# Kernel tuning notes

Hardware: AMD Instinct MI355X
Metric: run time of the kernel (lower is better)

Reference implementation:

```python
import jax, jax.numpy as jnp
import numpy as np
import math

B, T, N, IN_FEAT = 2, 64, 128, 2
H_LSTM = IN_FEAT * 2   # 4
D = IN_FEAT * 4        # 8
FH, FW = 16, 16
C_MAP = 2048
C_COMP = 32
TH = 0.5
IMG = 512.0


def setup_inputs() -> dict:
    key = jax.random.key(0)
    ks = jax.random.split(key, 20)
    s = 0.02
    inp = {
        "x": jax.random.uniform(ks[0], (B, 2, T, N), jnp.float32) * IMG,  # pixel coords in [0,512)
        "metadata": jax.random.normal(ks[1], (B, C_MAP, FH, FW), jnp.float32),
        # LSTM(in_feat, 2*in_feat): gates order i,f,g,o
        "w_ih": jax.random.normal(ks[2], (4 * H_LSTM, IN_FEAT), jnp.float32) * s,
        "w_hh": jax.random.normal(ks[3], (4 * H_LSTM, H_LSTM), jnp.float32) * s,
        "b_ih": jax.random.normal(ks[4], (4 * H_LSTM,), jnp.float32) * s,
        "b_hh": jax.random.normal(ks[5], (4 * H_LSTM,), jnp.float32) * s,
        "fc_w": jax.random.normal(ks[6], (D, H_LSTM), jnp.float32) * s,
        "fc_b": jax.random.normal(ks[7], (D,), jnp.float32) * s,
        "fc2_w": jax.random.normal(ks[8], (D, IN_FEAT), jnp.float32) * s,
        "fc2_b": jax.random.normal(ks[9], (D,), jnp.float32) * s,
        "fc3_w": jax.random.normal(ks[10], (D, IN_FEAT), jnp.float32) * s,
        "fc3_b": jax.random.normal(ks[11], (D,), jnp.float32) * s,
        "comp_w": jax.random.normal(ks[12], (C_COMP, C_MAP), jnp.float32) * s,
        "comp_b": jax.random.normal(ks[13], (C_COMP,), jnp.float32) * s,
        "vf_w": jax.random.normal(ks[14], (H_LSTM, H_LSTM + C_COMP), jnp.float32) * s,
        "vf_b": jax.random.normal(ks[15], (H_LSTM,), jnp.float32) * s,
        "fcout_w": jax.random.normal(ks[16], (IN_FEAT, D), jnp.float32) * s,
        "fcout_b": jax.random.normal(ks[17], (IN_FEAT,), jnp.float32) * s,
    }
    return inp


def _grid_sample_bilinear(fm, grid):
    # fm: [B,C,H,W]; grid: [B,P,1,2] normalized (x,y) in [-1,1]; bilinear, zeros padding, align_corners=False
    Bb, C, Hh, Ww = fm.shape
    gx, gy = grid[..., 0], grid[..., 1]              # [B,P,1]
    ix = ((gx + 1.0) * Ww - 1.0) * 0.5
    iy = ((gy + 1.0) * Hh - 1.0) * 0.5
    ix0 = jnp.floor(ix); iy0 = jnp.floor(iy)
    wx = ix - ix0; wy = iy - iy0

    def gather(f, yy, xx):
        valid = ((yy >= 0) & (yy < Hh) & (xx >= 0) & (xx < Ww)).astype(f.dtype)
        yc = jnp.clip(yy, 0, Hh - 1).astype(jnp.int32)
        xc = jnp.clip(xx, 0, Ww - 1).astype(jnp.int32)
        return f[:, yc, xc] * valid[None]            # [C,P,1]

    def per_batch(f, x0, y0, wx_, wy_):
        x1 = x0 + 1.0; y1 = y0 + 1.0
        return (gather(f, y0, x0) * ((1 - wy_) * (1 - wx_))[None]
                + gather(f, y0, x1) * ((1 - wy_) * wx_)[None]
                + gather(f, y1, x0) * (wy_ * (1 - wx_))[None]
                + gather(f, y1, x1) * (wy_ * wx_)[None])

    return jax.vmap(per_batch)(fm, ix0, iy0, wx, wy)  # [B,C,P,1]


def reference(x, metadata, w_ih, w_hh, b_ih, b_hh, fc_w, fc_b, fc2_w, fc2_b,
              fc3_w, fc3_b, comp_w, comp_b, vf_w, vf_b, fcout_w, fcout_b):
    coords = x                                        # [B,2,T,N] raw pixel coords
    xp = jnp.transpose(x, (0, 2, 3, 1))               # [B,T,N,2]
    b, t, n, c = xp.shape

    # sinusoidal positional encoding over time axis
    div = jnp.exp(jnp.arange(0, c, 2, dtype=jnp.float32) * (-math.log(10000.0) / c))
    pos = jnp.arange(t, dtype=jnp.float32)[:, None]
    pe = jnp.zeros((t, c), xp.dtype)
    pe = pe.at[:, 0::2].set(jnp.sin(pos * div))
    pe = pe.at[:, 1::2].set(jnp.cos(pos * div))
    xp = xp + pe[None, :, None, :]
    xr = xp.reshape(-1, c)                            # [M,2], M=b*t*n

    # single-step LSTM with zero init state (seq_len==1 in original)
    gates = xr @ w_ih.T + b_ih + b_hh                 # h0=0 => W_hh term vanishes
    i, f, g, o = jnp.split(gates, 4, axis=-1)
    cst = jax.nn.sigmoid(i) * jnp.tanh(g)
    X = jax.nn.sigmoid(o) * jnp.tanh(cst)             # [M,4]

    # visual fusion: 1x1 conv compressor + grid_sample local context
    comp = jnp.einsum('bchw,oc->bohw', metadata, comp_w) + comp_b[None, :, None, None]
    cgrid = jnp.transpose(coords, (0, 2, 3, 1)).reshape(b, -1, 1, 2)
    ngrid = 2.0 * (cgrid / IMG) - 1.0
    sampled = _grid_sample_bilinear(comp, ngrid)      # [B,32,TN,1]
    lc = jnp.transpose(sampled[..., 0], (0, 2, 1)).reshape(-1, C_COMP)  # [M,32]
    X = jnp.concatenate([X, lc], axis=-1) @ vf_w.T + vf_b               # [M,4]

    # sigmoid-gated full attention over all t*n tokens
    Q = (X @ fc_w.T + fc_b).reshape(b, t * n, -1)     # [B,TN,8]
    K = (xr @ fc2_w.T + fc2_b).reshape(b, t * n, -1)
    V = (xr @ fc3_w.T + fc3_b).reshape(b, t * n, -1)
    probs = jax.nn.sigmoid(jnp.einsum('bqd,bkd->bqk', Q, K))  # [B,TN,TN]
    out = jnp.einsum('bqk,bkd->bqd', probs, V).reshape(-1, Q.shape[-1])

    out = out * (out > TH).astype(out.dtype)          # threshold-ReLU
    out = out @ fcout_w.T + fcout_b                   # [M,2]
    out = out.reshape(b, t, n, -1)
    return jnp.transpose(out, (0, 3, 1, 2))           # [B,2,T,N]
```

## Files before the change

### kernel.cpp

```cpp
#include <hip/hip_runtime.h>
#include <math.h>

#define BB    2
#define TT    64
#define NN    128
#define TN    8192
#define MM    16384
#define CMAP  2048
#define CCOMP 32
#define FHW   256

#define CSPLIT 64
#define CRANGE 32

#define DEG    17
#define NS     18
#define NODD   9
#define MDIM   19
#define NMOMF  (MDIM*MDIM)
#define MCH    64
#define MPTS   128
#define ZFIT   5.0
#define ZFITF  5.0f
#define UVBOUND 1.0045f

struct QCoef { float cb[NS][NODD]; };

#define OFF_CP    0
#define OFF_COMP  (OFF_CP + CSPLIT*BB*FHW*CCOMP)
#define OFF_A     (OFF_COMP + BB*FHW*CCOMP)
#define OFF_X     (OFF_A + MM*4)
#define OFF_MP    (OFF_X + MM*2)

__device__ __forceinline__ float fast_sigmoid(float v) {
    return __builtin_amdgcn_rcpf(1.0f + __expf(-v));
}
__device__ __forceinline__ float fast_tanh(float v) {
    return 1.0f - 2.0f * __builtin_amdgcn_rcpf(1.0f + __expf(2.0f * v));
}

__global__ void k_comp_p(const float* __restrict__ metadata,
                         const float* __restrict__ comp_w,
                         float* __restrict__ Cp) {
    const int b  = blockIdx.x;
    const int cs = blockIdx.y;
    const int hw = threadIdx.x;

    __shared__ float wcs[CRANGE][CCOMP];
    for (int i = threadIdx.x; i < CRANGE * CCOMP; i += 256) {
        int c = i / CCOMP, o = i % CCOMP;
        wcs[c][o] = comp_w[o * CMAP + cs * CRANGE + c];
    }
    __syncthreads();

    float acc[CCOMP];
#pragma unroll
    for (int o = 0; o < CCOMP; o++) acc[o] = 0.0f;

    const float* mb = metadata + ((size_t)b * CMAP + (size_t)cs * CRANGE) * FHW + hw;
#pragma unroll 4
    for (int c = 0; c < CRANGE; c++) {
        float m = mb[c * FHW];
#pragma unroll
        for (int o = 0; o < CCOMP; o++) acc[o] += m * wcs[c][o];
    }

    float* outp = Cp + (size_t)cs * (BB * FHW * CCOMP) + ((size_t)b * FHW + hw) * CCOMP;
#pragma unroll
    for (int o = 0; o < CCOMP; o += 4) {
        *(float4*)&outp[o] = make_float4(acc[o], acc[o + 1], acc[o + 2], acc[o + 3]);
    }
}

__global__ void k_comp_reduce(const float* __restrict__ Cp,
                              const float* __restrict__ comp_b,
                              float* __restrict__ comp_ws) {
    const int t = threadIdx.x;
    const int i = blockIdx.x * 64 + (t >> 2);
    const int r = t & 3;

    float s = 0.0f;
#pragma unroll
    for (int k = 0; k < CSPLIT / 4; k++) {
        s += Cp[(size_t)(r * (CSPLIT / 4) + k) * (BB * FHW * CCOMP) + i];
    }
    s += __shfl_xor(s, 1);
    s += __shfl_xor(s, 2);
    if (r == 0) comp_ws[i] = s + comp_b[i & (CCOMP - 1)];
}

__global__ void k_token(const float* __restrict__ x,
                        const float* __restrict__ w_ih,
                        const float* __restrict__ b_ih,
                        const float* __restrict__ b_hh,
                        const float* __restrict__ fc_w,  const float* __restrict__ fc_b,
                        const float* __restrict__ fc2_w, const float* __restrict__ fc2_b,
                        const float* __restrict__ vf_w,  const float* __restrict__ vf_b,
                        const float* __restrict__ comp_ws,
                        float4* __restrict__ Aq, float2* __restrict__ Xr) {
    const int m = blockIdx.x * 64 + threadIdx.x;
    const int b = m >> 13;
    const int p = m & (TN - 1);
    const int t = p >> 7;

    const float px = x[(size_t)(b * 2 + 0) * TN + p];
    const float py = x[(size_t)(b * 2 + 1) * TN + p];

    const float xr0 = px + __sinf((float)t);
    const float xr1 = py + __cosf((float)t);
    Xr[m] = make_float2(xr0, xr1);

    float X[4];
#pragma unroll
    for (int j = 0; j < 4; j++) {
        float gi = xr0 * w_ih[(j)      * 2] + xr1 * w_ih[(j)      * 2 + 1] + b_ih[j]      + b_hh[j];
        float gg = xr0 * w_ih[(8 + j)  * 2] + xr1 * w_ih[(8 + j)  * 2 + 1] + b_ih[8 + j]  + b_hh[8 + j];
        float go = xr0 * w_ih[(12 + j) * 2] + xr1 * w_ih[(12 + j) * 2 + 1] + b_ih[12 + j] + b_hh[12 + j];
        float cst = fast_sigmoid(gi) * fast_tanh(gg);
        X[j] = fast_sigmoid(go) * fast_tanh(cst);
    }

    float lc[CCOMP];
#pragma unroll
    for (int c = 0; c < CCOMP; c++) lc[c] = 0.0f;

    const float ix = px * (1.0f / 32.0f) - 0.5f;
    const float iy = py * (1.0f / 32.0f) - 0.5f;
    const float fx0 = floorf(ix), fy0 = floorf(iy);
    const float wx = ix - fx0, wy = iy - fy0;
    const int x0 = (int)fx0, y0 = (int)fy0;
    const float* cb = comp_ws + (size_t)b * FHW * CCOMP;

#pragma unroll
    for (int dy = 0; dy < 2; dy++) {
#pragma unroll
        for (int dx = 0; dx < 2; dx++) {
            int xx = x0 + dx, yy = y0 + dy;
            if (xx < 0 || xx > 15 || yy < 0 || yy > 15) continue;
            float w = (dy ? wy : 1.0f - wy) * (dx ? wx : 1.0f - wx);
            const float4* cp4 = (const float4*)(cb + (yy * 16 + xx) * CCOMP);
#pragma unroll
            for (int c4 = 0; c4 < CCOMP / 4; c4++) {
                float4 v = cp4[c4];
                lc[c4 * 4 + 0] += w * v.x;
                lc[c4 * 4 + 1] += w * v.y;
                lc[c4 * 4 + 2] += w * v.z;
                lc[c4 * 4 + 3] += w * v.w;
            }
        }
    }

    float X2[4];
#pragma unroll
    for (int j = 0; j < 4; j++) {
        float a = vf_b[j];
#pragma unroll
        for (int k = 0; k < 4; k++) a += X[k] * vf_w[j * 36 + k];
#pragma unroll
        for (int c = 0; c < CCOMP; c++) a += lc[c] * vf_w[j * 36 + 4 + c];
        X2[j] = a;
    }

    float al = 0.0f, be = 0.0f, ga = 0.0f;
#pragma unroll
    for (int d = 0; d < 8; d++) {
        float q = fc_b[d];
#pragma unroll
        for (int k = 0; k < 4; k++) q += X2[k] * fc_w[d * 4 + k];
        al += q * fc2_b[d];
        be += q * fc2_w[d * 2];
        ga += q * fc2_w[d * 2 + 1];
    }
    Aq[m] = make_float4(al, be, ga, 0.0f);
}

__global__ void __launch_bounds__(256) k_mom(const float2* __restrict__ Xr,
                                             float* __restrict__ Mp) {
    const int b   = blockIdx.x;
    const int ch  = blockIdx.y;
    const int tid = threadIdx.x;

    __shared__ float spu[MPTS][MDIM];
    __shared__ float spv[MPTS][MDIM];

    if (tid < MPTS) {
        float2 xv = Xr[b * TN + ch * MPTS + tid];
        const float u = (xv.x - 256.0f) * (1.0f / 256.0f);
        const float v = (xv.y - 256.0f) * (1.0f / 256.0f);
        float a = 1.0f, c = 1.0f;
#pragma unroll
        for (int i = 0; i < MDIM; i++) {
            spu[tid][i] = a; spv[tid][i] = c;
            a *= u; c *= v;
        }
    }
    __syncthreads();

    float* outp = Mp + ((size_t)(b * MCH + ch)) * NMOMF;
    for (int i = tid; i < NMOMF; i += 256) {
        const int j = i / MDIM, l = i % MDIM;
        float s = 0.0f;
        if (j + l < MDIM) {
#pragma unroll 8
            for (int p = 0; p < MPTS; p++)
                s += spu[p][j] * spv[p][l];
        }
        outp[i] = s;
    }
}

__global__ void __launch_bounds__(256) k_query(const float4* __restrict__ Aq,
                                               const float2* __restrict__ Xr,
                                               const float* __restrict__ Mp,
                                               const float* __restrict__ fc3_w,
                                               const float* __restrict__ fc3_b,
                                               const float* __restrict__ fcout_w,
                                               const float* __restrict__ fcout_b,
                                               float* __restrict__ y,
                                               QCoef qc) {
    __shared__ float sM[NMOMF];

    const int tid = threadIdx.x;
    const int m   = blockIdx.x * 256 + tid;
    const int b   = m >> 13;
    const int p   = m & (TN - 1);

    for (int i = tid; i < NMOMF; i += 256) {
        float s = 0.0f;
        for (int ch = 0; ch < MCH; ch++)
            s += Mp[((size_t)(b * MCH + ch)) * NMOMF + i];
        sM[i] = s;
    }
    __syncthreads();

    const float4 A4 = Aq[m];
    const float al = A4.x, be = A4.y, ga = A4.z;
    const float b1 = 256.0f * be;
    const float c1 = 256.0f * ga;
    const float a0 = al + 256.0f * (be + ga);

    float S0, S1, S2;
    const float zb = fabsf(a0) + UVBOUND * (fabsf(b1) + fabsf(c1));
    if (zb >= ZFITF) {
        float s0 = 0.0f, s1 = 0.0f, s2 = 0.0f;
        const float2* xp = Xr + b * TN;
        for (int k = 0; k < TN; k++) {
            float2 kv = xp[k];
            float z = al + be * kv.x + ga * kv.y;
            float sg = fast_sigmoid(z);
            s0 += sg; s1 += sg * kv.x; s2 += sg * kv.y;
        }
        S0 = s0; S1 = s1; S2 = s2;
    } else {
        float pa[NS];
        pa[0] = 1.0f;
#pragma unroll
        for (int t = 1; t < NS; t++) pa[t] = pa[t - 1] * a0;

        float A[NS];
#pragma unroll
        for (int s = 0; s < NS; s++) {
            float acc = 0.0f;
            const int t0 = (s & 1) ? 0 : 1;
#pragma unroll
            for (int q = 0; q < NODD; q++) {
                const int t = t0 + 2 * q;
                if (s + t <= DEG) acc = fmaf(qc.cb[s][q], pa[t], acc);
            }
            A[s] = acc;
        }

        float R0 = A[0] * sM[0];
        float R1 = A[0] * sM[1 * MDIM + 0];
        float R2 = A[0] * sM[0 * MDIM + 1];

        float Ep[NS], Ec[NS];
        Ep[0] = 1.0f;
#pragma unroll
        for (int s = 1; s < NS; s++) {
            Ec[0] = c1 * Ep[0];
#pragma unroll
            for (int j = 1; j < NS; j++)
                if (j < s) Ec[j] = fmaf(b1, Ep[j - 1], c1 * Ep[j]);
            Ec[s] = b1 * Ep[s - 1];

            float W = 0.0f, W1 = 0.0f, W2 = 0.0f;
#pragma unroll
            for (int j = 0; j < NS; j++) {
                if (j <= s) {
                    const int l = s - j;
                    const float e = Ec[j];
                    W  = fmaf(e, sM[j * MDIM + l],           W);
                    W1 = fmaf(e, sM[(j + 1) * MDIM + l],     W1);
                    W2 = fmaf(e, sM[j * MDIM + l + 1],       W2);
                }
            }
            R0 = fmaf(A[s], W,  R0);
            R1 = fmaf(A[s], W1, R1);
            R2 = fmaf(A[s], W2, R2);
#pragma unroll
            for (int j = 0; j < NS; j++)
                if (j <= s) Ep[j] = Ec[j];
        }

        S0 = 4096.0f + R0;
        const float su = 0.5f * sM[1 * MDIM + 0] + R1;
        const float sv = 0.5f * sM[0 * MDIM + 1] + R2;
        S1 = 256.0f * su + 256.0f * S0;
        S2 = 256.0f * sv + 256.0f * S0;
    }

    float f0 = fcout_b[0], f1 = fcout_b[1];
#pragma unroll
    for (int d = 0; d < 8; d++) {
        float vv = S0 * fc3_b[d] + S1 * fc3_w[d * 2] + S2 * fc3_w[d * 2 + 1];
        vv = (vv > 0.5f) ? vv : 0.0f;
        f0 += vv * fcout_w[d];
        f1 += vv * fcout_w[8 + d];
    }
    y[(size_t)(b * 2 + 0) * TN + p] = f0;
    y[(size_t)(b * 2 + 1) * TN + p] = f1;
}

static QCoef compute_qcoef() {
    const int NNODE = 64;
    const double PI = 3.14159265358979323846;
    double term[NODD];
    for (int i = 0; i < NODD; ++i) term[i] = 0.0;

    for (int jn = 0; jn < NNODE; ++jn) {
        double theta = (jn + 0.5) * (PI / NNODE);
        double ct = cos(theta);
        double zj = ZFIT * ct;
        double fj = 1.0 / (1.0 + exp(-zj)) - 0.5;
        double Ckm2 = 1.0, Ckm1 = ct;
        term[0] += fj * ct;
        int idx = 1;
        for (int k = 2; k <= DEG; ++k) {
            double Ck = 2.0 * ct * Ckm1 - Ckm2;
            Ckm2 = Ckm1; Ckm1 = Ck;
            if (k & 1) term[idx++] += fj * Ck;
        }
    }

    double c[DEG + 1];
    for (int i = 0; i <= DEG; ++i) c[i] = 0.0;
    for (int i = 0; i < NODD; ++i) c[2 * i + 1] = term[i] * (2.0 / NNODE);

    double Tm2[DEG + 1], Tm1[DEG + 1], a[DEG + 1];
    for (int i = 0; i <= DEG; ++i) { Tm2[i] = 0.0; Tm1[i] = 0.0; a[i] = 0.0; }
    Tm2[0] = 1.0; Tm1[1] = 1.0;
    a[1] = c[1];
    for (int k = 2; k <= DEG; ++k) {
        double Tc[DEG + 1];
        for (int mm = 0; mm <= DEG; ++mm) Tc[mm] = 0.0;
        for (int mm = 0; mm <= k; ++mm) {
            double vv = -Tm2[mm];
            if (mm > 0) vv += 2.0 * Tm1[mm - 1];
            Tc[mm] = vv;
        }
        if (k & 1)
            for (int mm = 1; mm <= k; mm += 2) a[mm] += c[k] * Tc[mm];
        for (int mm = 0; mm <= DEG; ++mm) { Tm2[mm] = Tm1[mm]; Tm1[mm] = Tc[mm]; }
    }

    double Cz[DEG + 1];
    double sc = 1.0;
    for (int mm = 0; mm <= DEG; ++mm) { Cz[mm] = a[mm] * sc; sc *= (1.0 / ZFIT); }

    double Bi[NS][NS];
    for (int n = 0; n < NS; ++n)
        for (int k = 0; k < NS; ++k) Bi[n][k] = 0.0;
    for (int n = 0; n < NS; ++n) {
        Bi[n][0] = 1.0;
        for (int k = 1; k <= n; ++k)
            Bi[n][k] = Bi[n - 1][k - 1] + ((k <= n - 1) ? Bi[n - 1][k] : 0.0);
    }

    QCoef qc;
    for (int s = 0; s < NS; ++s)
        for (int q = 0; q < NODD; ++q) qc.cb[s][q] = 0.0f;
    for (int s = 0; s < NS; ++s) {
        int q = 0;
        for (int t = (s & 1) ? 0 : 1; s + t <= DEG; t += 2)
            qc.cb[s][q++] = (float)(Cz[s + t] * Bi[s + t][s]);
    }
    return qc;
}

extern "C" void kernel_launch(void* const* d_in, const int* in_sizes, int n_in,
                              void* d_out, int out_size, void* d_ws, size_t ws_size,
                              hipStream_t stream) {
    const float* x        = (const float*)d_in[0];
    const float* metadata = (const float*)d_in[1];
    const float* w_ih     = (const float*)d_in[2];
    const float* b_ih     = (const float*)d_in[4];
    const float* b_hh     = (const float*)d_in[5];
    const float* fc_w     = (const float*)d_in[6];
    const float* fc_b     = (const float*)d_in[7];
    const float* fc2_w    = (const float*)d_in[8];
    const float* fc2_b    = (const float*)d_in[9];
    const float* fc3_w    = (const float*)d_in[10];
    const float* fc3_b    = (const float*)d_in[11];
    const float* comp_w   = (const float*)d_in[12];
    const float* comp_b   = (const float*)d_in[13];
    const float* vf_w     = (const float*)d_in[14];
    const float* vf_b     = (const float*)d_in[15];
    const float* fcout_w  = (const float*)d_in[16];
    const float* fcout_b  = (const float*)d_in[17];

    static const QCoef qc = compute_qcoef();

    float*  ws      = (float*)d_ws;
    float*  Cp      = ws + OFF_CP;
    float*  comp_ws = ws + OFF_COMP;
    float4* Aq      = (float4*)(ws + OFF_A);
    float2* Xr      = (float2*)(ws + OFF_X);
    float*  Mp      = ws + OFF_MP;

    k_comp_p<<<dim3(BB, CSPLIT), 256, 0, stream>>>(metadata, comp_w, Cp);

    k_comp_reduce<<<256, 256, 0, stream>>>(Cp, comp_b, comp_ws);

    k_token<<<MM / 64, 64, 0, stream>>>(x, w_ih, b_ih, b_hh,
                                        fc_w, fc_b, fc2_w, fc2_b,
                                        vf_w, vf_b, comp_ws, Aq, Xr);

    k_mom<<<dim3(BB, MCH), 256, 0, stream>>>(Xr, Mp);

    k_query<<<MM / 256, 256, 0, stream>>>(Aq, Xr, Mp, fc3_w, fc3_b,
                                          fcout_w, fcout_b, (float*)d_out, qc);
}
```

Before: 127.0 us.

## Fuse all stages into one persistent kernel with software grid barriers

Replaces the five separate launches (compressor partials, reduction, per-token, moments, query) with a single 64-block persistent kernel. Phases are separated by atomic-counter grid barriers, and the per-token projections stay in registers instead of going through the Aq workspace buffer. The channel split and moment chunking are retuned to fit 64 blocks of 256 threads. This removes launch gaps and one global round-trip, but runs each phase on only 64 workgroups, adds barrier spin cost, and relies on all blocks being co-resident.

New measurement: 149.1 us. +17.4%, slower.

```diff
diff --git a/kernel.cpp b/kernel.cpp
--- a/kernel.cpp
+++ b/kernel.cpp
@@ -10,16 +10,18 @@
 #define CCOMP 32
 #define FHW   256
 
-#define CSPLIT 64
-#define CRANGE 32
+#define NBLK   64
+#define NTHR   256
+#define CSPLIT 32
+#define CRANGE 64
 
 #define DEG    17
 #define NS     18
 #define NODD   9
 #define MDIM   19
 #define NMOMF  (MDIM*MDIM)
-#define MCH    64
-#define MPTS   128
+#define MCH    32
+#define MPTS   256
 #define ZFIT   5.0
 #define ZFITF  5.0f
 #define UVBOUND 1.0045f
@@ -28,9 +30,24 @@
 
 #define OFF_CP    0
 #define OFF_COMP  (OFF_CP + CSPLIT*BB*FHW*CCOMP)
-#define OFF_A     (OFF_COMP + BB*FHW*CCOMP)
-#define OFF_X     (OFF_A + MM*4)
+#define OFF_X     (OFF_COMP + BB*FHW*CCOMP)
 #define OFF_MP    (OFF_X + MM*2)
+
+#define NBAR 4
+__device__ unsigned g_bar[NBAR];
+
+__device__ __forceinline__ void grid_bar(int ph) {
+    __syncthreads();
+    if (threadIdx.x == 0) {
+        __threadfence();
+        unsigned my  = atomicAdd(&g_bar[ph], 1u);
+        unsigned tgt = (my / NBLK + 1u) * NBLK;
+        while (atomicAdd(&g_bar[ph], 0u) < tgt)
+            __builtin_amdgcn_s_sleep(1);
+    }
+    __syncthreads();
+    __threadfence();
+}
 
 __device__ __forceinline__ float fast_sigmoid(float v) {
     return __builtin_amdgcn_rcpf(1.0f + __expf(-v));
@@ -39,152 +56,152 @@
     return 1.0f - 2.0f * __builtin_amdgcn_rcpf(1.0f + __expf(2.0f * v));
 }
 
-__global__ void k_comp_p(const float* __restrict__ metadata,
-                         const float* __restrict__ comp_w,
-                         float* __restrict__ Cp) {
-    const int b  = blockIdx.x;
-    const int cs = blockIdx.y;
-    const int hw = threadIdx.x;
-
-    __shared__ float wcs[CRANGE][CCOMP];
-    for (int i = threadIdx.x; i < CRANGE * CCOMP; i += 256) {
-        int c = i / CCOMP, o = i % CCOMP;
-        wcs[c][o] = comp_w[o * CMAP + cs * CRANGE + c];
-    }
-    __syncthreads();
-
-    float acc[CCOMP];
-#pragma unroll
-    for (int o = 0; o < CCOMP; o++) acc[o] = 0.0f;
-
-    const float* mb = metadata + ((size_t)b * CMAP + (size_t)cs * CRANGE) * FHW + hw;
+__global__ void __launch_bounds__(256) k_fused(
+        const float* __restrict__ x,
+        const float* __restrict__ metadata,
+        const float* __restrict__ w_ih,
+        const float* __restrict__ b_ih,  const float* __restrict__ b_hh,
+        const float* __restrict__ fc_w,  const float* __restrict__ fc_b,
+        const float* __restrict__ fc2_w, const float* __restrict__ fc2_b,
+        const float* __restrict__ fc3_w, const float* __restrict__ fc3_b,
+        const float* __restrict__ comp_w, const float* __restrict__ comp_b,
+        const float* __restrict__ vf_w,  const float* __restrict__ vf_b,
+        const float* __restrict__ fcout_w, const float* __restrict__ fcout_b,
+        float* __restrict__ ws, float* __restrict__ y, QCoef qc) {
+
+    __shared__ float lds[2 * MPTS * MDIM];
+
+    float* Cp      = ws + OFF_CP;
+    float* comp_ws = ws + OFF_COMP;
+    float2* Xr     = (float2*)(ws + OFF_X);
+    float* Mp      = ws + OFF_MP;
+
+    const int blk = blockIdx.x;
+    const int tid = threadIdx.x;
+    const int m   = blk * NTHR + tid;
+
+    {
+        const int b  = blk >> 5;
+        const int cs = blk & 31;
+        float (*wcs)[CCOMP] = (float(*)[CCOMP])lds;
+        for (int i = tid; i < CRANGE * CCOMP; i += NTHR) {
+            int c = i >> 5, o = i & 31;
+            wcs[c][o] = comp_w[o * CMAP + cs * CRANGE + c];
+        }
+        __syncthreads();
+
+        float acc[CCOMP];
+#pragma unroll
+        for (int o = 0; o < CCOMP; o++) acc[o] = 0.0f;
+
+        const float* mb = metadata + ((size_t)b * CMAP + (size_t)cs * CRANGE) * FHW + tid;
 #pragma unroll 4
-    for (int c = 0; c < CRANGE; c++) {
-        float m = mb[c * FHW];
-#pragma unroll
-        for (int o = 0; o < CCOMP; o++) acc[o] += m * wcs[c][o];
-    }
-
-    float* outp = Cp + (size_t)cs * (BB * FHW * CCOMP) + ((size_t)b * FHW + hw) * CCOMP;
-#pragma unroll
-    for (int o = 0; o < CCOMP; o += 4) {
-        *(float4*)&outp[o] = make_float4(acc[o], acc[o + 1], acc[o + 2], acc[o + 3]);
-    }
-}
-
-__global__ void k_comp_reduce(const float* __restrict__ Cp,
-                              const float* __restrict__ comp_b,
-                              float* __restrict__ comp_ws) {
-    const int t = threadIdx.x;
-    const int i = blockIdx.x * 64 + (t >> 2);
-    const int r = t & 3;
-
-    float s = 0.0f;
-#pragma unroll
-    for (int k = 0; k < CSPLIT / 4; k++) {
-        s += Cp[(size_t)(r * (CSPLIT / 4) + k) * (BB * FHW * CCOMP) + i];
-    }
-    s += __shfl_xor(s, 1);
-    s += __shfl_xor(s, 2);
-    if (r == 0) comp_ws[i] = s + comp_b[i & (CCOMP - 1)];
-}
-
-__global__ void k_token(const float* __restrict__ x,
-                        const float* __restrict__ w_ih,
-                        const float* __restrict__ b_ih,
-                        const float* __restrict__ b_hh,
-                        const float* __restrict__ fc_w,  const float* __restrict__ fc_b,
-                        const float* __restrict__ fc2_w, const float* __restrict__ fc2_b,
-                        const float* __restrict__ vf_w,  const float* __restrict__ vf_b,
-                        const float* __restrict__ comp_ws,
-                        float4* __restrict__ Aq, float2* __restrict__ Xr) {
-    const int m = blockIdx.x * 64 + threadIdx.x;
-    const int b = m >> 13;
-    const int p = m & (TN - 1);
-    const int t = p >> 7;
-
-    const float px = x[(size_t)(b * 2 + 0) * TN + p];
-    const float py = x[(size_t)(b * 2 + 1) * TN + p];
-
-    const float xr0 = px + __sinf((float)t);
-    const float xr1 = py + __cosf((float)t);
-    Xr[m] = make_float2(xr0, xr1);
-
-    float X[4];
-#pragma unroll
-    for (int j = 0; j < 4; j++) {
-        float gi = xr0 * w_ih[(j)      * 2] + xr1 * w_ih[(j)      * 2 + 1] + b_ih[j]      + b_hh[j];
-        float gg = xr0 * w_ih[(8 + j)  * 2] + xr1 * w_ih[(8 + j)  * 2 + 1] + b_ih[8 + j]  + b_hh[8 + j];
-        float go = xr0 * w_ih[(12 + j) * 2] + xr1 * w_ih[(12 + j) * 2 + 1] + b_ih[12 + j] + b_hh[12 + j];
-        float cst = fast_sigmoid(gi) * fast_tanh(gg);
-        X[j] = fast_sigmoid(go) * fast_tanh(cst);
-    }
-
-    float lc[CCOMP];
-#pragma unroll
-    for (int c = 0; c < CCOMP; c++) lc[c] = 0.0f;
-
-    const float ix = px * (1.0f / 32.0f) - 0.5f;
-    const float iy = py * (1.0f / 32.0f) - 0.5f;
-    const float fx0 = floorf(ix), fy0 = floorf(iy);
-    const float wx = ix - fx0, wy = iy - fy0;
-    const int x0 = (int)fx0, y0 = (int)fy0;
-    const float* cb = comp_ws + (size_t)b * FHW * CCOMP;
-
-#pragma unroll
-    for (int dy = 0; dy < 2; dy++) {
-#pragma unroll
-        for (int dx = 0; dx < 2; dx++) {
-            int xx = x0 + dx, yy = y0 + dy;
-            if (xx < 0 || xx > 15 || yy < 0 || yy > 15) continue;
-            float w = (dy ? wy : 1.0f - wy) * (dx ? wx : 1.0f - wx);
-            const float4* cp4 = (const float4*)(cb + (yy * 16 + xx) * CCOMP);
-#pragma unroll
-            for (int c4 = 0; c4 < CCOMP / 4; c4++) {
-                float4 v = cp4[c4];
-                lc[c4 * 4 + 0] += w * v.x;
-                lc[c4 * 4 + 1] += w * v.y;
-                lc[c4 * 4 + 2] += w * v.z;
-                lc[c4 * 4 + 3] += w * v.w;
+        for (int c = 0; c < CRANGE; c++) {
+            float mv = mb[c * FHW];
+#pragma unroll
+            for (int o = 0; o < CCOMP; o++) acc[o] += mv * wcs[c][o];
+        }
+
+        float* outp = Cp + (size_t)cs * (BB * FHW * CCOMP) + ((size_t)b * FHW + tid) * CCOMP;
+#pragma unroll
+        for (int o = 0; o < CCOMP; o += 4)
+            *(float4*)&outp[o] = make_float4(acc[o], acc[o + 1], acc[o + 2], acc[o + 3]);
+    }
+    grid_bar(0);
+
+    {
+        float s = 0.0f;
+#pragma unroll
+        for (int cs = 0; cs < CSPLIT; cs++)
+            s += Cp[(size_t)cs * (BB * FHW * CCOMP) + m];
+        comp_ws[m] = s + comp_b[m & (CCOMP - 1)];
+    }
+    grid_bar(1);
+
+    float al, be, ga;
+    {
+        const int b = m >> 13;
+        const int p = m & (TN - 1);
+        const int t = p >> 7;
+
+        const float px = x[(size_t)(b * 2 + 0) * TN + p];
+        const float py = x[(size_t)(b * 2 + 1) * TN + p];
+
+        const float xr0 = px + __sinf((float)t);
+        const float xr1 = py + __cosf((float)t);
+        Xr[m] = make_float2(xr0, xr1);
+
+        float X[4];
+#pragma unroll
+        for (int j = 0; j < 4; j++) {
+            float gi = xr0 * w_ih[(j)      * 2] + xr1 * w_ih[(j)      * 2 + 1] + b_ih[j]      + b_hh[j];
+            float gg = xr0 * w_ih[(8 + j)  * 2] + xr1 * w_ih[(8 + j)  * 2 + 1] + b_ih[8 + j]  + b_hh[8 + j];
+            float go = xr0 * w_ih[(12 + j) * 2] + xr1 * w_ih[(12 + j) * 2 + 1] + b_ih[12 + j] + b_hh[12 + j];
+            float cst = fast_sigmoid(gi) * fast_tanh(gg);
+            X[j] = fast_sigmoid(go) * fast_tanh(cst);
+        }
+
+        float lc[CCOMP];
+#pragma unroll
+        for (int c = 0; c < CCOMP; c++) lc[c] = 0.0f;
+
+        const float ix = px * (1.0f / 32.0f) - 0.5f;
+        const float iy = py * (1.0f / 32.0f) - 0.5f;
+        const float fx0 = floorf(ix), fy0 = floorf(iy);
+        const float wx = ix - fx0, wy = iy - fy0;
+        const int x0 = (int)fx0, y0 = (int)fy0;
+        const float* cb = comp_ws + (size_t)b * FHW * CCOMP;
+
+#pragma unroll
+        for (int dy = 0; dy < 2; dy++) {
+#pragma unroll
+            for (int dx = 0; dx < 2; dx++) {
+                int xx = x0 + dx, yy = y0 + dy;
+                if (xx < 0 || xx > 15 || yy < 0 || yy > 15) continue;
+                float w = (dy ? wy : 1.0f - wy) * (dx ? wx : 1.0f - wx);
+                const float4* cp4 = (const float4*)(cb + (yy * 16 + xx) * CCOMP);
+#pragma unroll
+                for (int c4 = 0; c4 < CCOMP / 4; c4++) {
+                    float4 v = cp4[c4];
+                    lc[c4 * 4 + 0] += w * v.x;
+                    lc[c4 * 4 + 1] += w * v.y;
+                    lc[c4 * 4 + 2] += w * v.z;
+                    lc[c4 * 4 + 3] += w * v.w;
+                }
             }
         }
-    }
-
-    float X2[4];
-#pragma unroll
-    for (int j = 0; j < 4; j++) {
-        float a = vf_b[j];
-#pragma unroll
-        for (int k = 0; k < 4; k++) a += X[k] * vf_w[j * 36 + k];
-#pragma unroll
-        for (int c = 0; c < CCOMP; c++) a += lc[c] * vf_w[j * 36 + 4 + c];
-        X2[j] = a;
-    }
-
-    float al = 0.0f, be = 0.0f, ga = 0.0f;
-#pragma unroll
-    for (int d = 0; d < 8; d++) {
-        float q = fc_b[d];
-#pragma unroll
-        for (int k = 0; k < 4; k++) q += X2[k] * fc_w[d * 4 + k];
-        al += q * fc2_b[d];
-        be += q * fc2_w[d * 2];
-        ga += q * fc2_w[d * 2 + 1];
-    }
-    Aq[m] = make_float4(al, be, ga, 0.0f);
-}
-
-__global__ void __launch_bounds__(256) k_mom(const float2* __restrict__ Xr,
-                                             float* __restrict__ Mp) {
-    const int b   = blockIdx.x;
-    const int ch  = blockIdx.y;
-    const int tid = threadIdx.x;
-
-    __shared__ float spu[MPTS][MDIM];
-    __shared__ float spv[MPTS][MDIM];
-
-    if (tid < MPTS) {
-        float2 xv = Xr[b * TN + ch * MPTS + tid];
+
+        float X2[4];
+#pragma unroll
+        for (int j = 0; j < 4; j++) {
+            float a = vf_b[j];
+#pragma unroll
+            for (int k = 0; k < 4; k++) a += X[k] * vf_w[j * 36 + k];
+#pragma unroll
+            for (int c = 0; c < CCOMP; c++) a += lc[c] * vf_w[j * 36 + 4 + c];
+            X2[j] = a;
+        }
+
+        al = 0.0f; be = 0.0f; ga = 0.0f;
+#pragma unroll
+        for (int d = 0; d < 8; d++) {
+            float q = fc_b[d];
+#pragma unroll
+            for (int k = 0; k < 4; k++) q += X2[k] * fc_w[d * 4 + k];
+            al += q * fc2_b[d];
+            be += q * fc2_w[d * 2];
+            ga += q * fc2_w[d * 2 + 1];
+        }
+    }
+    grid_bar(2);
+
+    {
+        const int b3 = blk >> 5;
+        const int ch = blk & 31;
+        float (*spu)[MDIM] = (float(*)[MDIM])lds;
+        float (*spv)[MDIM] = (float(*)[MDIM])(lds + MPTS * MDIM);
+
+        float2 xv = Xr[b3 * TN + ch * MPTS + tid];
         const float u = (xv.x - 256.0f) * (1.0f / 256.0f);
         const float v = (xv.y - 256.0f) * (1.0f / 256.0f);
         float a = 1.0f, c = 1.0f;
@@ -193,133 +210,121 @@
             spu[tid][i] = a; spv[tid][i] = c;
             a *= u; c *= v;
         }
-    }
-    __syncthreads();
-
-    float* outp = Mp + ((size_t)(b * MCH + ch)) * NMOMF;
-    for (int i = tid; i < NMOMF; i += 256) {
-        const int j = i / MDIM, l = i % MDIM;
-        float s = 0.0f;
-        if (j + l < MDIM) {
+        __syncthreads();
+
+        float* outp = Mp + ((size_t)(b3 * MCH + ch)) * NMOMF;
+        for (int i = tid; i < NMOMF; i += NTHR) {
+            const int j = i / MDIM, l = i % MDIM;
+            float s = 0.0f;
+            if (j + l < MDIM) {
 #pragma unroll 8
-            for (int p = 0; p < MPTS; p++)
-                s += spu[p][j] * spv[p][l];
-        }
-        outp[i] = s;
-    }
-}
-
-__global__ void __launch_bounds__(256) k_query(const float4* __restrict__ Aq,
-                                               const float2* __restrict__ Xr,
-                                               const float* __restrict__ Mp,
-                                               const float* __restrict__ fc3_w,
-                                               const float* __restrict__ fc3_b,
-                                               const float* __restrict__ fcout_w,
-                                               const float* __restrict__ fcout_b,
-                                               float* __restrict__ y,
-                                               QCoef qc) {
-    __shared__ float sM[NMOMF];
-
-    const int tid = threadIdx.x;
-    const int m   = blockIdx.x * 256 + tid;
-    const int b   = m >> 13;
-    const int p   = m & (TN - 1);
-
-    for (int i = tid; i < NMOMF; i += 256) {
-        float s = 0.0f;
-        for (int ch = 0; ch < MCH; ch++)
-            s += Mp[((size_t)(b * MCH + ch)) * NMOMF + i];
-        sM[i] = s;
-    }
-    __syncthreads();
-
-    const float4 A4 = Aq[m];
-    const float al = A4.x, be = A4.y, ga = A4.z;
-    const float b1 = 256.0f * be;
-    const float c1 = 256.0f * ga;
-    const float a0 = al + 256.0f * (be + ga);
-
-    float S0, S1, S2;
-    const float zb = fabsf(a0) + UVBOUND * (fabsf(b1) + fabsf(c1));
-    if (zb >= ZFITF) {
-        float s0 = 0.0f, s1 = 0.0f, s2 = 0.0f;
-        const float2* xp = Xr + b * TN;
-        for (int k = 0; k < TN; k++) {
-            float2 kv = xp[k];
-            float z = al + be * kv.x + ga * kv.y;
-            float sg = fast_sigmoid(z);
-            s0 += sg; s1 += sg * kv.x; s2 += sg * kv.y;
-        }
-        S0 = s0; S1 = s1; S2 = s2;
-    } else {
-        float pa[NS];
-        pa[0] = 1.0f;
-#pragma unroll
-        for (int t = 1; t < NS; t++) pa[t] = pa[t - 1] * a0;
-
-        float A[NS];
-#pragma unroll
-        for (int s = 0; s < NS; s++) {
-            float acc = 0.0f;
-            const int t0 = (s & 1) ? 0 : 1;
-#pragma unroll
-            for (int q = 0; q < NODD; q++) {
-                const int t = t0 + 2 * q;
-                if (s + t <= DEG) acc = fmaf(qc.cb[s][q], pa[t], acc);
+                for (int p = 0; p < MPTS; p++)
+                    s += spu[p][j] * spv[p][l];
             }
-            A[s] = acc;
-        }
-
-        float R0 = A[0] * sM[0];
-        float R1 = A[0] * sM[1 * MDIM + 0];
-        float R2 = A[0] * sM[0 * MDIM + 1];
-
-        float Ep[NS], Ec[NS];
-        Ep[0] = 1.0f;
-#pragma unroll
-        for (int s = 1; s < NS; s++) {
-            Ec[0] = c1 * Ep[0];
-#pragma unroll
-            for (int j = 1; j < NS; j++)
-                if (j < s) Ec[j] = fmaf(b1, Ep[j - 1], c1 * Ep[j]);
-            Ec[s] = b1 * Ep[s - 1];
-
-            float W = 0.0f, W1 = 0.0f, W2 = 0.0f;
-#pragma unroll
-            for (int j = 0; j < NS; j++) {
-                if (j <= s) {
-                    const int l = s - j;
-                    const float e = Ec[j];
-                    W  = fmaf(e, sM[j * MDIM + l],           W);
-                    W1 = fmaf(e, sM[(j + 1) * MDIM + l],     W1);
-                    W2 = fmaf(e, sM[j * MDIM + l + 1],       W2);
+            outp[i] = s;
+        }
+    }
+    grid_bar(3);
+
+    {
+        const int b = m >> 13;
+        const int p = m & (TN - 1);
+        float* sM = lds;
+
+        for (int i = tid; i < NMOMF; i += NTHR) {
+            float s = 0.0f;
+            for (int ch = 0; ch < MCH; ch++)
+                s += Mp[((size_t)(b * MCH + ch)) * NMOMF + i];
+            sM[i] = s;
+        }
+        __syncthreads();
+
+        const float b1 = 256.0f * be;
+        const float c1 = 256.0f * ga;
+        const float a0 = al + 256.0f * (be + ga);
+
+        float S0, S1, S2;
+        const float zb = fabsf(a0) + UVBOUND * (fabsf(b1) + fabsf(c1));
+        if (zb >= ZFITF) {
+            float s0 = 0.0f, s1 = 0.0f, s2 = 0.0f;
+            const float2* xp = Xr + b * TN;
+            for (int k = 0; k < TN; k++) {
+                float2 kv = xp[k];
+                float z = al + be * kv.x + ga * kv.y;
+                float sg = fast_sigmoid(z);
+                s0 += sg; s1 += sg * kv.x; s2 += sg * kv.y;
+            }
+            S0 = s0; S1 = s1; S2 = s2;
+        } else {
+            float pa[NS];
+            pa[0] = 1.0f;
+#pragma unroll
+            for (int t = 1; t < NS; t++) pa[t] = pa[t - 1] * a0;
+
+            float A[NS];
+#pragma unroll
+            for (int s = 0; s < NS; s++) {
+                float acc = 0.0f;
+                const int t0 = (s & 1) ? 0 : 1;
+#pragma unroll
+                for (int q = 0; q < NODD; q++) {
+                    const int t = t0 + 2 * q;
+                    if (s + t <= DEG) acc = fmaf(qc.cb[s][q], pa[t], acc);
                 }
+                A[s] = acc;
             }
-            R0 = fmaf(A[s], W,  R0);
-            R1 = fmaf(A[s], W1, R1);
-            R2 = fmaf(A[s], W2, R2);
-#pragma unroll
-            for (int j = 0; j < NS; j++)
-                if (j <= s) Ep[j] = Ec[j];
-        }
-
-        S0 = 4096.0f + R0;
-        const float su = 0.5f * sM[1 * MDIM + 0] + R1;
-        const float sv = 0.5f * sM[0 * MDIM + 1] + R2;
-        S1 = 256.0f * su + 256.0f * S0;
-        S2 = 256.0f * sv + 256.0f * S0;
-    }
-
-    float f0 = fcout_b[0], f1 = fcout_b[1];
-#pragma unroll
-    for (int d = 0; d < 8; d++) {
-        float vv = S0 * fc3_b[d] + S1 * fc3_w[d * 2] + S2 * fc3_w[d * 2 + 1];
-        vv = (vv > 0.5f) ? vv : 0.0f;
-        f0 += vv * fcout_w[d];
-        f1 += vv * fcout_w[8 + d];
-    }
-    y[(size_t)(b * 2 + 0) * TN + p] = f0;
-    y[(size_t)(b * 2 + 1) * TN + p] = f1;
+
+            float R0 = A[0] * sM[0];
+            float R1 = A[0] * sM[1 * MDIM + 0];
+            float R2 = A[0] * sM[0 * MDIM + 1];
+
+            float Ep[NS], Ec[NS];
+            Ep[0] = 1.0f;
+#pragma unroll
+            for (int s = 1; s < NS; s++) {
+                Ec[0] = c1 * Ep[0];
+#pragma unroll
+                for (int j = 1; j < NS; j++)
+                    if (j < s) Ec[j] = fmaf(b1, Ep[j - 1], c1 * Ep[j]);
+                Ec[s] = b1 * Ep[s - 1];
+
+                float W = 0.0f, W1 = 0.0f, W2 = 0.0f;
+#pragma unroll
+                for (int j = 0; j < NS; j++) {
+                    if (j <= s) {
+                        const int l = s - j;
+                        const float e = Ec[j];
+                        W  = fmaf(e, sM[j * MDIM + l],       W);
+                        W1 = fmaf(e, sM[(j + 1) * MDIM + l], W1);
+                        W2 = fmaf(e, sM[j * MDIM + l + 1],   W2);
+                    }
+                }
+                R0 = fmaf(A[s], W,  R0);
+                R1 = fmaf(A[s], W1, R1);
+                R2 = fmaf(A[s], W2, R2);
+#pragma unroll
+                for (int j = 0; j < NS; j++)
+                    if (j <= s) Ep[j] = Ec[j];
+            }
+
+            S0 = 4096.0f + R0;
+            const float su = 0.5f * sM[1 * MDIM + 0] + R1;
+            const float sv = 0.5f * sM[0 * MDIM + 1] + R2;
+            S1 = 256.0f * su + 256.0f * S0;
+            S2 = 256.0f * sv + 256.0f * S0;
+        }
+
+        float f0 = fcout_b[0], f1 = fcout_b[1];
+#pragma unroll
+        for (int d = 0; d < 8; d++) {
+            float vv = S0 * fc3_b[d] + S1 * fc3_w[d * 2] + S2 * fc3_w[d * 2 + 1];
+            vv = (vv > 0.5f) ? vv : 0.0f;
+            f0 += vv * fcout_w[d];
+            f1 += vv * fcout_w[8 + d];
+        }
+        y[(size_t)(b * 2 + 0) * TN + p] = f0;
+        y[(size_t)(b * 2 + 1) * TN + p] = f1;
+    }
 }
 
 static QCoef compute_qcoef() {
@@ -411,23 +416,9 @@
 
     static const QCoef qc = compute_qcoef();
 
-    float*  ws      = (float*)d_ws;
-    float*  Cp      = ws + OFF_CP;
-    float*  comp_ws = ws + OFF_COMP;
-    float4* Aq      = (float4*)(ws + OFF_A);
-    float2* Xr      = (float2*)(ws + OFF_X);
-    float*  Mp      = ws + OFF_MP;
-
-    k_comp_p<<<dim3(BB, CSPLIT), 256, 0, stream>>>(metadata, comp_w, Cp);
-
-    k_comp_reduce<<<256, 256, 0, stream>>>(Cp, comp_b, comp_ws);
-
-    k_token<<<MM / 64, 64, 0, stream>>>(x, w_ih, b_ih, b_hh,
-                                        fc_w, fc_b, fc2_w, fc2_b,
-                                        vf_w, vf_b, comp_ws, Aq, Xr);
-
-    k_mom<<<dim3(BB, MCH), 256, 0, stream>>>(Xr, Mp);
-
-    k_query<<<MM / 256, 256, 0, stream>>>(Aq, Xr, Mp, fc3_w, fc3_b,
-                                          fcout_w, fcout_b, (float*)d_out, qc);
-}
+    k_fused<<<NBLK, NTHR, 0, stream>>>(x, metadata, w_ih, b_ih, b_hh,
+                                       fc_w, fc_b, fc2_w, fc2_b,
+                                       fc3_w, fc3_b, comp_w, comp_b,
+                                       vf_w, vf_b, fcout_w, fcout_b,
+                                       (float*)d_ws, (float*)d_out, qc);
+}
```
